# Kernel tuning notes

Hardware: AMD Instinct MI355X
Metric: run time of the kernel (lower is better)

## Reference

```python
import jax, jax.numpy as jnp
import numpy as np

R = 16
LORA_ALPHA = 16
SCALING = LORA_ALPHA / R  # 1.0


def setup_inputs() -> dict:
    key = jax.random.key(0)
    kx, kr, ka = jax.random.split(key, 3)
    B, S, D, DO, E = 4, 2048, 4096, 4096, 8
    x = jax.random.normal(kx, (B, S, D), dtype=jnp.float32)
    # kaiming_uniform_(a=sqrt(5)) on Linear weight of fan_in=D -> U(-1/sqrt(D), 1/sqrt(D))
    bound_r = 1.0 / np.sqrt(D)
    route_w = jax.random.uniform(kr, (E, D), jnp.float32, -bound_r, bound_r)  # lora_route.weight
    bound_a = 1.0 / np.sqrt(D)
    A = jax.random.uniform(ka, (E, R, D), jnp.float32, -bound_a, bound_a)  # stacked lora_A{i}.weight [r, D]
    # lora_B weights are zero-initialized in the module; use small random for a nontrivial baseline
    kb = jax.random.fold_in(key, 7)
    Bw = jax.random.normal(kb, (E, DO, R), dtype=jnp.float32) * 0.02  # stacked lora_B{i}.weight [DO, r]
    return {"x": x, "route_w": route_w, "A": A, "Bw": Bw}


def reference(x, route_w, A, Bw):
    # router logits [B, S, E]
    logits = jnp.einsum("bsd,ed->bse", x, route_w)
    # top-1 hard routing: keep raw logit value at the argmax slot, zero elsewhere
    topk_v, topk_idx = jax.lax.top_k(logits, 1)  # [B,S,1]
    E = logits.shape[-1]
    route_weight = jax.nn.one_hot(topk_idx[..., 0], E, dtype=logits.dtype) * topk_v  # [B,S,E]
    # low-rank per-expert projections (dense over experts, as in the original loop)
    h = jnp.einsum("bsd,erd->bser", x, A)            # [B,S,E,r]
    wh = route_weight[..., None] * h                  # weight before the up-projection
    out = jnp.einsum("bser,eor->bso", wh, Bw) * SCALING  # [B,S,DO]
    return out
```

## Files before the change

kernel.cpp:

```cpp
#include <hip/hip_runtime.h>
#include <hip/hip_bf16.h>

#define DD   4096
#define NE   8
#define NR   16
#define NTOK 8192
#define NDO  4096
#define TAU  4e-4f
#define MAXFLAG 8000

typedef __attribute__((ext_vector_type(8))) __bf16 bf16x8;
typedef __attribute__((ext_vector_type(4))) float  f32x4;

__device__ __forceinline__ bf16x8 to_bf16x8(float4 a, float4 b) {
    bf16x8 r;
    r[0] = (__bf16)a.x; r[1] = (__bf16)a.y; r[2] = (__bf16)a.z; r[3] = (__bf16)a.w;
    r[4] = (__bf16)b.x; r[5] = (__bf16)b.y; r[6] = (__bf16)b.z; r[7] = (__bf16)b.w;
    return r;
}

__device__ __forceinline__ bf16x8 lo_bf16x8(float4 a, float4 b, bf16x8 h) {
    bf16x8 r;
    r[0] = (__bf16)(a.x - (float)h[0]); r[1] = (__bf16)(a.y - (float)h[1]);
    r[2] = (__bf16)(a.z - (float)h[2]); r[3] = (__bf16)(a.w - (float)h[3]);
    r[4] = (__bf16)(b.x - (float)h[4]); r[5] = (__bf16)(b.y - (float)h[5]);
    r[6] = (__bf16)(b.z - (float)h[6]); r[7] = (__bf16)(b.w - (float)h[7]);
    return r;
}

__global__ __launch_bounds__(1024) void k_route(const float* __restrict__ x,
                                                const float* __restrict__ rw,
                                                float* __restrict__ w_arr,
                                                int*   __restrict__ token_list,
                                                int*   __restrict__ count,
                                                int*   __restrict__ nflag,
                                                int*   __restrict__ flaglist) {
    const int t0   = blockIdx.x * 16;
    const int wv   = threadIdx.x >> 6;
    const int lane = threadIdx.x & 63;
    const int m    = lane & 15;
    const int half = lane >> 4;

    const float* xrow = x + (size_t)(t0 + m) * DD;
    const float* wrow = rw + (size_t)(m & 7) * DD;
    const bool   blo  = (m >> 3) != 0;

    f32x4 accH = {0.f,0.f,0.f,0.f}, accL = {0.f,0.f,0.f,0.f};
    const int kbase = wv * 256;
    #pragma unroll
    for (int ks = 0; ks < 8; ks++) {
        const int k0 = kbase + ks * 32 + half * 8;
        const float4 xa = *(const float4*)(xrow + k0);
        const float4 xb = *(const float4*)(xrow + k0 + 4);
        const float4 wa = *(const float4*)(wrow + k0);
        const float4 wb = *(const float4*)(wrow + k0 + 4);
        const bf16x8 xh = to_bf16x8(xa, xb);
        const bf16x8 xl = lo_bf16x8(xa, xb, xh);
        const bf16x8 wh = to_bf16x8(wa, wb);
        const bf16x8 bfrag = blo ? lo_bf16x8(wa, wb, wh) : wh;
        accH = __builtin_amdgcn_mfma_f32_16x16x32_bf16(xh, bfrag, accH, 0, 0, 0);
        accL = __builtin_amdgcn_mfma_f32_16x16x32_bf16(xl, bfrag, accL, 0, 0, 0);
    }

    __shared__ float Lred[16][16][17];
    #pragma unroll
    for (int r = 0; r < 4; r++)
        Lred[wv][half * 4 + r][m] = accH[r] + accL[r];
    __syncthreads();

    __shared__ float logit[16][NE];
    if (threadIdx.x < 128) {
        const int t = threadIdx.x >> 3, ee = threadIdx.x & 7;
        float s = 0.f;
        #pragma unroll
        for (int w = 0; w < 16; w++) s += Lred[w][t][ee] + Lred[w][t][ee + 8];
        logit[t][ee] = s;
    }
    __syncthreads();

    if (threadIdx.x < 16) {
        const int t = threadIdx.x;
        float best = -1e30f, second = -1e30f; int be = 0;
        #pragma unroll
        for (int e = 0; e < NE; e++) {
            const float s = logit[t][e];
            if (s > best) { second = best; best = s; be = e; }
            else if (s > second) { second = s; }
        }
        const int tok = t0 + t;
        w_arr[tok] = best;
        if (best - second < TAU) {
            const int p = atomicAdd(nflag, 1);
            if (p < MAXFLAG) flaglist[p] = tok;
        } else {
            const int p = atomicAdd(&count[be], 1);
            token_list[be * NTOK + p] = tok;
        }
    }
}

__global__ __launch_bounds__(256) void k_fix(const float* __restrict__ x,
                                             const float* __restrict__ rw,
                                             float* __restrict__ w_arr,
                                             int*   __restrict__ token_list,
                                             int*   __restrict__ count,
                                             const int* __restrict__ nflag,
                                             const int* __restrict__ flaglist) {
    const int wv   = threadIdx.x >> 6;
    const int lane = threadIdx.x & 63;
    int n = *nflag; if (n > MAXFLAG) n = MAXFLAG;

    for (int idx = blockIdx.x * 4 + wv; idx < n; idx += 128) {
        const int tok = flaglist[idx];
        const float* xp = x + (size_t)tok * DD;
        double acc[NE];
        #pragma unroll
        for (int e = 0; e < NE; e++) acc[e] = 0.0;
        for (int i = 0; i < 16; i++) {
            const int d4 = (i * 64 + lane) * 4;
            const float4 xv = *(const float4*)(xp + d4);
            const double x0 = xv.x, x1 = xv.y, x2 = xv.z, x3 = xv.w;
            #pragma unroll
            for (int e = 0; e < NE; e++) {
                const float4 wv4 = *(const float4*)(rw + (size_t)e * DD + d4);
                acc[e] = fma(x0, (double)wv4.x, acc[e]);
                acc[e] = fma(x1, (double)wv4.y, acc[e]);
                acc[e] = fma(x2, (double)wv4.z, acc[e]);
                acc[e] = fma(x3, (double)wv4.w, acc[e]);
            }
        }
        #pragma unroll
        for (int off = 32; off > 0; off >>= 1)
            #pragma unroll
            for (int e = 0; e < NE; e++)
                acc[e] += __shfl_xor(acc[e], off, 64);
        if (lane == 0) {
            double best = acc[0]; int be = 0;
            #pragma unroll
            for (int e = 1; e < NE; e++) if (acc[e] > best) { best = acc[e]; be = e; }
            w_arr[tok] = (float)best;
            const int pos = atomicAdd(&count[be], 1);
            token_list[be * NTOK + pos] = tok;
        }
    }
}

__global__ __launch_bounds__(1024) void k_h(const float* __restrict__ x,
                                            const float* __restrict__ Am,
                                            const float* __restrict__ w_arr,
                                            const int*   __restrict__ token_list,
                                            const int*   __restrict__ count,
                                            __hip_bfloat16* __restrict__ wh) {
    const int e    = blockIdx.x >> 7;
    const int g    = blockIdx.x & 127;
    const int cnt  = count[e];
    const int base = g * 32;
    if (base >= cnt) return;

    const int wv   = threadIdx.x >> 6;
    const int lane = threadIdx.x & 63;
    const int m    = lane & 15;
    const int half = lane >> 4;

    const int i0 = base + m,  i1 = base + 16 + m;
    const int tok0 = (i0 < cnt) ? token_list[e * NTOK + i0] : 0;
    const int tok1 = (i1 < cnt) ? token_list[e * NTOK + i1] : 0;
    const float* xr0  = x + (size_t)tok0 * DD;
    const float* xr1  = x + (size_t)tok1 * DD;
    const float* arow = Am + ((size_t)e * NR + m) * DD;

    f32x4 acc0 = {0.f,0.f,0.f,0.f}, acc1 = {0.f,0.f,0.f,0.f};
    const int kbase = wv * 256;
    #pragma unroll
    for (int kc = 0; kc < 8; kc++) {
        const int k0 = kbase + kc * 32 + half * 8;
        const bf16x8 bfrag = to_bf16x8(*(const float4*)(arow + k0),
                                       *(const float4*)(arow + k0 + 4));
        const bf16x8 a0 = to_bf16x8(*(const float4*)(xr0 + k0),
                                    *(const float4*)(xr0 + k0 + 4));
        const bf16x8 a1 = to_bf16x8(*(const float4*)(xr1 + k0),
                                    *(const float4*)(xr1 + k0 + 4));
        acc0 = __builtin_amdgcn_mfma_f32_16x16x32_bf16(a0, bfrag, acc0, 0, 0, 0);
        acc1 = __builtin_amdgcn_mfma_f32_16x16x32_bf16(a1, bfrag, acc1, 0, 0, 0);
    }

    __shared__ float lds[16][32][17];
    #pragma unroll
    for (int rr = 0; rr < 4; rr++) {
        lds[wv][half * 4 + rr][m]      = acc0[rr];
        lds[wv][16 + half * 4 + rr][m] = acc1[rr];
    }
    __syncthreads();

    if (threadIdx.x < 512) {
        const int t = threadIdx.x >> 4;
        const int r = threadIdx.x & 15;
        const int i2 = base + t;
        if (i2 < cnt) {
            float s = 0.f;
            #pragma unroll
            for (int w = 0; w < 16; w++) s += lds[w][t][r];
            const int tk = token_list[e * NTOK + i2];
            wh[(size_t)tk * NR + r] = (__hip_bfloat16)(s * w_arr[tk]);
        }
    }
}

__global__ __launch_bounds__(256) void k_out(const float* __restrict__ Bw,
                                             const __hip_bfloat16* __restrict__ wh,
                                             const int*   __restrict__ token_list,
                                             const int*   __restrict__ count,
                                             float* __restrict__ out) {
    const int bx    = blockIdx.x;
    const int chunk = bx & 3;
    const int slot  = (bx >> 2) & 511;
    const int e     = bx >> 11;
    const int cnt   = count[e];
    const int base  = slot * 16;
    if (base >= cnt) return;

    const int wv   = threadIdx.x >> 6;
    const int lane = threadIdx.x & 63;
    const int m    = lane & 15;
    const int half = lane >> 4;

    const int  idx   = base + m;
    const bool valid = idx < cnt;
    const int  tok   = valid ? token_list[e * NTOK + idx] : 0;

    bf16x8 a2;
    if (half < 2 && valid) {
        a2 = *(const bf16x8*)(wh + (size_t)tok * NR + half * 8);
    } else {
        #pragma unroll
        for (int j = 0; j < 8; j++) a2[j] = (__bf16)0.0f;
    }

    int trow[4]; bool vrow[4];
    #pragma unroll
    for (int r = 0; r < 4; r++) {
        const int ir = base + half * 4 + r;
        vrow[r] = ir < cnt;
        trow[r] = vrow[r] ? token_list[e * NTOK + ir] : 0;
    }

    const float* bwe = Bw + (size_t)e * NDO * NR;
    const int h2 = (half < 2) ? half : 0;
    const f32x4 zero4 = {0.f, 0.f, 0.f, 0.f};
    const int ob0 = chunk * 1024 + wv * 256;

    #pragma unroll 4
    for (int ot = 0; ot < 16; ot++) {
        const int obase = ob0 + ot * 16;
        const float* bp = bwe + (size_t)(obase + m) * NR + h2 * 8;
        const float4 p = *(const float4*)(bp);
        const float4 q = *(const float4*)(bp + 4);
        bf16x8 b2 = to_bf16x8(p, q);
        if (half >= 2) {
            #pragma unroll
            for (int j = 0; j < 8; j++) b2[j] = (__bf16)0.0f;
        }
        const f32x4 d = __builtin_amdgcn_mfma_f32_16x16x32_bf16(a2, b2, zero4, 0, 0, 0);
        #pragma unroll
        for (int r = 0; r < 4; r++) {
            if (vrow[r]) out[(size_t)trow[r] * NDO + obase + m] = d[r];
        }
    }
}

extern "C" void kernel_launch(void* const* d_in, const int* in_sizes, int n_in,
                              void* d_out, int out_size, void* d_ws, size_t ws_size,
                              hipStream_t stream) {
    const float* x  = (const float*)d_in[0];
    const float* rw = (const float*)d_in[1];
    const float* Am = (const float*)d_in[2];
    const float* Bw = (const float*)d_in[3];
    float* out = (float*)d_out;

    char* ws = (char*)d_ws;
    int*   count      = (int*)ws;
    int*   nflag      = (int*)(ws + 32);
    float* w_arr      = (float*)(ws + 512);
    int*   flaglist   = (int*)(ws + 33280);
    int*   token_list = (int*)(ws + 65536);
    __hip_bfloat16* wh = (__hip_bfloat16*)(ws + 65536 + NE * NTOK * 4);

    hipMemsetAsync(ws, 0, 64, stream);
    hipLaunchKernelGGL(k_route, dim3(512),   dim3(1024), 0, stream, x, rw, w_arr, token_list, count, nflag, flaglist);
    hipLaunchKernelGGL(k_fix,   dim3(32),    dim3(256),  0, stream, x, rw, w_arr, token_list, count, nflag, flaglist);
    hipLaunchKernelGGL(k_h,     dim3(1024),  dim3(1024), 0, stream, x, Am, w_arr, token_list, count, wh);
    hipLaunchKernelGGL(k_out,   dim3(16384), dim3(256),  0, stream, Bw, wh, token_list, count, out);
}
```

Measured before the change: 170.6 us.

## Precast inputs to bf16 once and route with single-pass bf16 MFMA

A new prep kernel converts x, A, Bw and a hi/lo split of the router weights to bf16 in workspace. The routing, h and output kernels then load bf16 directly instead of converting fp32 on every load. Routing drops from two MFMAs (x hi and x lo) to one, which loses precision on x. To compensate, the near-tie threshold TAU is raised so more tokens go to the fp64 fix kernel, which now launches more blocks. This adds an extra full pass writing a bf16 copy of x, and fix-path work rises with the larger threshold.

```diff
diff --git a/kernel.cpp b/kernel.cpp
--- a/kernel.cpp
+++ b/kernel.cpp
@@ -6,7 +6,7 @@
 #define NR   16
 #define NTOK 8192
 #define NDO  4096
-#define TAU  4e-4f
+#define TAU  0.01f
 #define MAXFLAG 8000
 
 typedef __attribute__((ext_vector_type(8))) __bf16 bf16x8;
@@ -28,8 +28,56 @@
     return r;
 }
 
-__global__ __launch_bounds__(1024) void k_route(const float* __restrict__ x,
-                                                const float* __restrict__ rw,
+__device__ __forceinline__ bf16x8 zero_frag() {
+    bf16x8 z;
+    #pragma unroll
+    for (int j = 0; j < 8; j++) z[j] = (__bf16)0.0f;
+    return z;
+}
+
+__global__ __launch_bounds__(256) void k_prep(const float* __restrict__ x,
+                                              const float* __restrict__ rw,
+                                              const float* __restrict__ Am,
+                                              const float* __restrict__ Bw,
+                                              __bf16* __restrict__ xb,
+                                              __bf16* __restrict__ rwhl,
+                                              __bf16* __restrict__ Ab,
+                                              __bf16* __restrict__ Bwb) {
+    const int b = blockIdx.x;
+    const float* src;  __bf16* dst;  size_t base;
+    if (b < 4096)      { base = (size_t)b * 8192 + threadIdx.x * 32;            src = x;  dst = xb;  }
+    else if (b < 4160) { base = (size_t)(b - 4096) * 8192 + threadIdx.x * 32;   src = Am; dst = Ab;  }
+    else if (b < 4224) { base = (size_t)(b - 4160) * 8192 + threadIdx.x * 32;   src = Bw; dst = Bwb; }
+    else {
+        const int obase = (b - 4224) * 8192 + threadIdx.x * 32;
+        const int row = obase >> 12, k = obase & 4095;
+        const float* s = rw + ((size_t)(row & 7) << 12) + k;
+        float4 v[8];
+        #pragma unroll
+        for (int i = 0; i < 8; i++) v[i] = *(const float4*)(s + i * 4);
+        if (row < 8) {
+            #pragma unroll
+            for (int i = 0; i < 4; i++)
+                *(bf16x8*)(rwhl + obase + i * 8) = to_bf16x8(v[2*i], v[2*i+1]);
+        } else {
+            #pragma unroll
+            for (int i = 0; i < 4; i++) {
+                const bf16x8 h = to_bf16x8(v[2*i], v[2*i+1]);
+                *(bf16x8*)(rwhl + obase + i * 8) = lo_bf16x8(v[2*i], v[2*i+1], h);
+            }
+        }
+        return;
+    }
+    float4 v[8];
+    #pragma unroll
+    for (int i = 0; i < 8; i++) v[i] = *(const float4*)(src + base + i * 4);
+    #pragma unroll
+    for (int i = 0; i < 4; i++)
+        *(bf16x8*)(dst + base + i * 8) = to_bf16x8(v[2*i], v[2*i+1]);
+}
+
+__global__ __launch_bounds__(1024) void k_route(const __bf16* __restrict__ xb,
+                                                const __bf16* __restrict__ rwhl,
                                                 float* __restrict__ w_arr,
                                                 int*   __restrict__ token_list,
                                                 int*   __restrict__ count,
@@ -41,40 +89,32 @@
     const int m    = lane & 15;
     const int half = lane >> 4;
 
-    const float* xrow = x + (size_t)(t0 + m) * DD;
-    const float* wrow = rw + (size_t)(m & 7) * DD;
-    const bool   blo  = (m >> 3) != 0;
-
-    f32x4 accH = {0.f,0.f,0.f,0.f}, accL = {0.f,0.f,0.f,0.f};
+    const __bf16* xrow = xb   + (size_t)(t0 + m) * DD;
+    const __bf16* wrow = rwhl + (size_t)m * DD;
+
+    f32x4 acc = {0.f, 0.f, 0.f, 0.f};
     const int kbase = wv * 256;
     #pragma unroll
     for (int ks = 0; ks < 8; ks++) {
         const int k0 = kbase + ks * 32 + half * 8;
-        const float4 xa = *(const float4*)(xrow + k0);
-        const float4 xb = *(const float4*)(xrow + k0 + 4);
-        const float4 wa = *(const float4*)(wrow + k0);
-        const float4 wb = *(const float4*)(wrow + k0 + 4);
-        const bf16x8 xh = to_bf16x8(xa, xb);
-        const bf16x8 xl = lo_bf16x8(xa, xb, xh);
-        const bf16x8 wh = to_bf16x8(wa, wb);
-        const bf16x8 bfrag = blo ? lo_bf16x8(wa, wb, wh) : wh;
-        accH = __builtin_amdgcn_mfma_f32_16x16x32_bf16(xh, bfrag, accH, 0, 0, 0);
-        accL = __builtin_amdgcn_mfma_f32_16x16x32_bf16(xl, bfrag, accL, 0, 0, 0);
+        const bf16x8 a = *(const bf16x8*)(xrow + k0);
+        const bf16x8 b = *(const bf16x8*)(wrow + k0);
+        acc = __builtin_amdgcn_mfma_f32_16x16x32_bf16(a, b, acc, 0, 0, 0);
     }
 
     __shared__ float Lred[16][16][17];
     #pragma unroll
     for (int r = 0; r < 4; r++)
-        Lred[wv][half * 4 + r][m] = accH[r] + accL[r];
+        Lred[wv][half * 4 + r][m] = acc[r];
     __syncthreads();
 
-    __shared__ float logit[16][NE];
+    __shared__ float logitS[16][NE];
     if (threadIdx.x < 128) {
         const int t = threadIdx.x >> 3, ee = threadIdx.x & 7;
         float s = 0.f;
         #pragma unroll
         for (int w = 0; w < 16; w++) s += Lred[w][t][ee] + Lred[w][t][ee + 8];
-        logit[t][ee] = s;
+        logitS[t][ee] = s;
     }
     __syncthreads();
 
@@ -83,7 +123,7 @@
         float best = -1e30f, second = -1e30f; int be = 0;
         #pragma unroll
         for (int e = 0; e < NE; e++) {
-            const float s = logit[t][e];
+            const float s = logitS[t][e];
             if (s > best) { second = best; best = s; be = e; }
             else if (s > second) { second = s; }
         }
@@ -110,7 +150,7 @@
     const int lane = threadIdx.x & 63;
     int n = *nflag; if (n > MAXFLAG) n = MAXFLAG;
 
-    for (int idx = blockIdx.x * 4 + wv; idx < n; idx += 128) {
+    for (int idx = blockIdx.x * 4 + wv; idx < n; idx += 512) {
         const int tok = flaglist[idx];
         const float* xp = x + (size_t)tok * DD;
         double acc[NE];
@@ -145,8 +185,8 @@
     }
 }
 
-__global__ __launch_bounds__(1024) void k_h(const float* __restrict__ x,
-                                            const float* __restrict__ Am,
+__global__ __launch_bounds__(1024) void k_h(const __bf16* __restrict__ xb,
+                                            const __bf16* __restrict__ Ab,
                                             const float* __restrict__ w_arr,
                                             const int*   __restrict__ token_list,
                                             const int*   __restrict__ count,
@@ -165,21 +205,18 @@
     const int i0 = base + m,  i1 = base + 16 + m;
     const int tok0 = (i0 < cnt) ? token_list[e * NTOK + i0] : 0;
     const int tok1 = (i1 < cnt) ? token_list[e * NTOK + i1] : 0;
-    const float* xr0  = x + (size_t)tok0 * DD;
-    const float* xr1  = x + (size_t)tok1 * DD;
-    const float* arow = Am + ((size_t)e * NR + m) * DD;
+    const __bf16* xr0  = xb + (size_t)tok0 * DD;
+    const __bf16* xr1  = xb + (size_t)tok1 * DD;
+    const __bf16* arow = Ab + ((size_t)e * NR + m) * DD;
 
     f32x4 acc0 = {0.f,0.f,0.f,0.f}, acc1 = {0.f,0.f,0.f,0.f};
     const int kbase = wv * 256;
     #pragma unroll
     for (int kc = 0; kc < 8; kc++) {
         const int k0 = kbase + kc * 32 + half * 8;
-        const bf16x8 bfrag = to_bf16x8(*(const float4*)(arow + k0),
-                                       *(const float4*)(arow + k0 + 4));
-        const bf16x8 a0 = to_bf16x8(*(const float4*)(xr0 + k0),
-                                    *(const float4*)(xr0 + k0 + 4));
-        const bf16x8 a1 = to_bf16x8(*(const float4*)(xr1 + k0),
-                                    *(const float4*)(xr1 + k0 + 4));
+        const bf16x8 bfrag = *(const bf16x8*)(arow + k0);
+        const bf16x8 a0    = *(const bf16x8*)(xr0 + k0);
+        const bf16x8 a1    = *(const bf16x8*)(xr1 + k0);
         acc0 = __builtin_amdgcn_mfma_f32_16x16x32_bf16(a0, bfrag, acc0, 0, 0, 0);
         acc1 = __builtin_amdgcn_mfma_f32_16x16x32_bf16(a1, bfrag, acc1, 0, 0, 0);
     }
@@ -206,7 +243,7 @@
     }
 }
 
-__global__ __launch_bounds__(256) void k_out(const float* __restrict__ Bw,
+__global__ __launch_bounds__(256) void k_out(const __bf16* __restrict__ Bwb,
                                              const __hip_bfloat16* __restrict__ wh,
                                              const int*   __restrict__ token_list,
                                              const int*   __restrict__ count,
@@ -227,14 +264,11 @@
     const int  idx   = base + m;
     const bool valid = idx < cnt;
     const int  tok   = valid ? token_list[e * NTOK + idx] : 0;
-
-    bf16x8 a2;
-    if (half < 2 && valid) {
-        a2 = *(const bf16x8*)(wh + (size_t)tok * NR + half * 8);
-    } else {
-        #pragma unroll
-        for (int j = 0; j < 8; j++) a2[j] = (__bf16)0.0f;
-    }
+    const bf16x8 zf  = zero_frag();
+
+    bf16x8 a2 = (half < 2 && valid)
+        ? *(const bf16x8*)((const __bf16*)wh + (size_t)tok * NR + half * 8)
+        : zf;
 
     int trow[4]; bool vrow[4];
     #pragma unroll
@@ -244,7 +278,7 @@
         trow[r] = vrow[r] ? token_list[e * NTOK + ir] : 0;
     }
 
-    const float* bwe = Bw + (size_t)e * NDO * NR;
+    const __bf16* bwe = Bwb + (size_t)e * NDO * NR;
     const int h2 = (half < 2) ? half : 0;
     const f32x4 zero4 = {0.f, 0.f, 0.f, 0.f};
     const int ob0 = chunk * 1024 + wv * 256;
@@ -252,14 +286,9 @@
     #pragma unroll 4
     for (int ot = 0; ot < 16; ot++) {
         const int obase = ob0 + ot * 16;
-        const float* bp = bwe + (size_t)(obase + m) * NR + h2 * 8;
-        const float4 p = *(const float4*)(bp);
-        const float4 q = *(const float4*)(bp + 4);
-        bf16x8 b2 = to_bf16x8(p, q);
-        if (half >= 2) {
-            #pragma unroll
-            for (int j = 0; j < 8; j++) b2[j] = (__bf16)0.0f;
-        }
+        const bf16x8 b2 = (half < 2)
+            ? *(const bf16x8*)(bwe + (size_t)(obase + m) * NR + h2 * 8)
+            : zf;
         const f32x4 d = __builtin_amdgcn_mfma_f32_16x16x32_bf16(a2, b2, zero4, 0, 0, 0);
         #pragma unroll
         for (int r = 0; r < 4; r++) {
@@ -283,11 +312,16 @@
     float* w_arr      = (float*)(ws + 512);
     int*   flaglist   = (int*)(ws + 33280);
     int*   token_list = (int*)(ws + 65536);
-    __hip_bfloat16* wh = (__hip_bfloat16*)(ws + 65536 + NE * NTOK * 4);
+    __hip_bfloat16* wh = (__hip_bfloat16*)(ws + 327680);
+    __bf16* rwhl      = (__bf16*)(ws + 589824);
+    __bf16* Bwb       = (__bf16*)(ws + 720896);
+    __bf16* Ab        = (__bf16*)(ws + 1769472);
+    __bf16* xb        = (__bf16*)(ws + 4194304);
 
     hipMemsetAsync(ws, 0, 64, stream);
-    hipLaunchKernelGGL(k_route, dim3(512),   dim3(1024), 0, stream, x, rw, w_arr, token_list, count, nflag, flaglist);
-    hipLaunchKernelGGL(k_fix,   dim3(32),    dim3(256),  0, stream, x, rw, w_arr, token_list, count, nflag, flaglist);
-    hipLaunchKernelGGL(k_h,     dim3(1024),  dim3(1024), 0, stream, x, Am, w_arr, token_list, count, wh);
-    hipLaunchKernelGGL(k_out,   dim3(16384), dim3(256),  0, stream, Bw, wh, token_list, count, out);
-}
+    hipLaunchKernelGGL(k_prep,  dim3(4232),  dim3(256),  0, stream, x, rw, Am, Bw, xb, rwhl, Ab, Bwb);
+    hipLaunchKernelGGL(k_route, dim3(512),   dim3(1024), 0, stream, xb, rwhl, w_arr, token_list, count, nflag, flaglist);
+    hipLaunchKernelGGL(k_fix,   dim3(128),   dim3(256),  0, stream, x, rw, w_arr, token_list, count, nflag, flaglist);
+    hipLaunchKernelGGL(k_h,     dim3(1024),  dim3(1024), 0, stream, xb, Ab, w_arr, token_list, count, wh);
+    hipLaunchKernelGGL(k_out,   dim3(16384), dim3(256),  0, stream, Bwb, wh, token_list, count, out);
+}
```

New measurement: 172.0 us. Within noise of the previous version (+0.8%).
